# Optimization experiments

Measured on AMD Instinct MI355X. Metric: run time of the kernel, lower is better.

The kernel has to match this reference:

```python
import jax, jax.numpy as jnp
import numpy as np

D_MODEL = 1024
N_HEADS = 16
HEAD_DIM = D_MODEL // N_HEADS


def setup_inputs() -> dict:
    key = jax.random.key(0)
    ks = jax.random.split(key, 7)
    b, s, l = 2, 2048, 8
    x = jax.random.normal(ks[0], (b, s, D_MODEL), dtype=jnp.float32)
    past_keys = jax.random.normal(ks[1], (b, N_HEADS, s, l, HEAD_DIM), dtype=jnp.float32)
    past_values = jax.random.normal(ks[2], (b, N_HEADS, s, l, HEAD_DIM), dtype=jnp.float32)
    sc = 1.0 / np.sqrt(D_MODEL)
    W_qkv = jax.random.normal(ks[3], (D_MODEL, 3 * D_MODEL), dtype=jnp.float32) * sc
    b_qkv = jnp.zeros((3 * D_MODEL,), dtype=jnp.float32)
    W_out = jax.random.normal(ks[4], (D_MODEL, D_MODEL), dtype=jnp.float32) * sc
    b_out = jnp.zeros((D_MODEL,), dtype=jnp.float32)
    return {"x": x, "past_keys": past_keys, "past_values": past_values,
            "W_qkv": W_qkv, "b_qkv": b_qkv, "W_out": W_out, "b_out": b_out}


def _split_heads(t):
    b, s, d = t.shape
    return t.reshape(b, s, N_HEADS, HEAD_DIM).transpose(0, 2, 1, 3)  # [b,h,s,hd]


def reference(x, past_keys, past_values, W_qkv, b_qkv, W_out, b_out):
    b, s, _ = x.shape
    qkv = x @ W_qkv + b_qkv  # [b,s,3d]
    q_row, k_row, v_row = jnp.split(qkv, 3, axis=-1)
    q = _split_heads(q_row)  # [b,h,s,hd]
    k = _split_heads(k_row)
    v = _split_heads(v_row)
    scale = 1.0 / jnp.sqrt(jnp.asarray(HEAD_DIM, dtype=x.dtype))
    token_scores = jnp.einsum('bhqd,bhkd->bhqk', q, k) * scale  # [b,h,s,s]
    causal = jnp.triu(jnp.ones((s, s), dtype=bool), k=1)
    token_scores = jnp.where(causal, -jnp.inf, token_scores)
    mem_scores = jnp.einsum('bhsd,bhsld->bhsl', q, past_keys) * scale  # [b,h,s,l]
    scores = jnp.concatenate([token_scores, mem_scores], axis=-1)  # [b,h,s,s+l]
    weights = jax.nn.softmax(scores, axis=-1)
    token_w = weights[..., :s]
    mem_w = weights[..., s:]
    token_ctx = jnp.einsum('bhqk,bhkd->bhqd', token_w, v)
    mem_ctx = jnp.einsum('bhsl,bhsld->bhsd', mem_w, past_values)
    out = token_ctx + mem_ctx  # [b,h,s,hd]
    out = out.transpose(0, 2, 1, 3).reshape(b, s, D_MODEL)
    out = out @ W_out + b_out
    return out, k, v
```

## Files before the change

### kernel.cpp

```cpp
#include <hip/hip_runtime.h>
#include <hip/hip_bf16.h>

#define D_MODEL 1024
#define N_HEADS 16
#define HEAD_DIM 64
#define BATCH 2
#define SEQ 2048
#define NMEM 8

#define SCALE_L2 0.18033688f

typedef __attribute__((ext_vector_type(8))) short vshort8;
typedef __attribute__((ext_vector_type(4))) short vshort4;
typedef __attribute__((ext_vector_type(4))) float f32x4;

static __device__ __forceinline__ short f2bf(float f) {
    unsigned u = __builtin_bit_cast(unsigned, f);
    unsigned r = u + 0x7fffu + ((u >> 16) & 1u);
    return (short)(r >> 16);
}
static __device__ __forceinline__ float bf2f(short s) {
    unsigned u = ((unsigned)(unsigned short)s) << 16;
    return __builtin_bit_cast(float, u);
}

static __device__ __forceinline__ f32x4 mfma16x16x32(vshort8 a, vshort8 b, f32x4 c) {
    return __builtin_amdgcn_mfma_f32_16x16x32_bf16(a, b, c, 0, 0, 0);
}

typedef const __attribute__((address_space(1))) char* gptr_t;
typedef __attribute__((address_space(3))) char* lptr_t;
static __device__ __forceinline__ void gload_lds16(const void* g, void* l) {
    __builtin_amdgcn_global_load_lds((gptr_t)g, (lptr_t)l, 16, 0, 0);
}

__global__ void cast_f32_bf16(const float* __restrict__ in, short* __restrict__ out, int n4) {
    int i = blockIdx.x * blockDim.x + threadIdx.x;
    if (i >= n4) return;
    float4 v = reinterpret_cast<const float4*>(in)[i];
    vshort4 o;
    o.x = f2bf(v.x); o.y = f2bf(v.y); o.z = f2bf(v.z); o.w = f2bf(v.w);
    reinterpret_cast<vshort4*>(out)[i] = o;
}

__global__ void transpose_cast(const float* __restrict__ in, short* __restrict__ out, int R, int C) {
    __shared__ float tile[32][33];
    int n0 = blockIdx.x * 32;
    int k0 = blockIdx.y * 32;
    int tx = threadIdx.x, ty = threadIdx.y;
    #pragma unroll
    for (int i = 0; i < 4; i++) {
        int r = ty + i * 8;
        tile[r][tx] = in[(k0 + r) * C + n0 + tx];
    }
    __syncthreads();
    #pragma unroll
    for (int i = 0; i < 4; i++) {
        int r = ty + i * 8;
        out[(n0 + r) * R + k0 + tx] = f2bf(tile[tx][r]);
    }
}

#define BM 128
#define BN 128
#define BK 64

template<int EPI>
__global__ __launch_bounds__(256) void gemm_bf16(
    const short* __restrict__ A, const short* __restrict__ Bt,
    int M, int N, int K,
    const float* __restrict__ bias,
    float* __restrict__ Cout,
    short* __restrict__ Qb, short* __restrict__ Kb, short* __restrict__ Vt,
    float* __restrict__ k_out, float* __restrict__ v_out)
{
    __shared__ short As[BM][BK];
    __shared__ short Bs[BN][BK];
    int m0 = blockIdx.x * BM, n0 = blockIdx.y * BN;
    int tid = threadIdx.x;
    int wave = tid >> 6, lane = tid & 63;
    int wr = wave >> 1, wc = wave & 1;
    int lo = lane & 15, hi = lane >> 4;

    f32x4 acc[4][4];
    #pragma unroll
    for (int i = 0; i < 4; i++)
        #pragma unroll
        for (int j = 0; j < 4; j++)
            acc[i][j] = (f32x4){0.f, 0.f, 0.f, 0.f};

    int srow8 = wave * 8 + (lane >> 3);
    const char* Ab = (const char*)&As[0][0];
    const char* Bb = (const char*)&Bs[0][0];

    for (int k0 = 0; k0 < K; k0 += BK) {
        __syncthreads();
        #pragma unroll
        for (int r = 0; r < 4; r++) {
            int row = r * 32 + srow8;
            int sc8 = (((lane & 7) ^ (row & 7)) << 3);
            size_t dstoff = (size_t)r * 4096 + wave * 1024 + (size_t)(lane & 63) * 16;
            gload_lds16(&A[(size_t)(m0 + row) * K + k0 + sc8], (char*)Ab + dstoff);
            gload_lds16(&Bt[(size_t)(n0 + row) * K + k0 + sc8], (char*)Bb + dstoff);
        }
        __syncthreads();
        #pragma unroll
        for (int kk = 0; kk < 2; kk++) {
            vshort8 av[4], bv[4];
            #pragma unroll
            for (int fr = 0; fr < 4; fr++) {
                int ra = wr * 64 + fr * 16 + lo;
                av[fr] = *reinterpret_cast<const vshort8*>(
                    Ab + ra * 128 + (((kk * 4 + hi) ^ (ra & 7)) << 4));
            }
            #pragma unroll
            for (int fc = 0; fc < 4; fc++) {
                int rb = wc * 64 + fc * 16 + lo;
                bv[fc] = *reinterpret_cast<const vshort8*>(
                    Bb + rb * 128 + (((kk * 4 + hi) ^ (rb & 7)) << 4));
            }
            #pragma unroll
            for (int fr = 0; fr < 4; fr++)
                #pragma unroll
                for (int fc = 0; fc < 4; fc++)
                    acc[fr][fc] = mfma16x16x32(av[fr], bv[fc], acc[fr][fc]);
        }
    }

    #pragma unroll
    for (int fr = 0; fr < 4; fr++) {
        #pragma unroll
        for (int fc = 0; fc < 4; fc++) {
            int col = n0 + wc * 64 + fc * 16 + lo;
            float bb = bias[col];
            #pragma unroll
            for (int j = 0; j < 4; j++) {
                int row = m0 + wr * 64 + fr * 16 + hi * 4 + j;
                float val = acc[fr][fc][j] + bb;
                if (EPI == 0) {
                    Cout[row * N + col] = val;
                } else {
                    int sec = col >> 10, c = col & 1023;
                    int h = c >> 6, d = c & 63;
                    int b = row >> 11, s = row & 2047;
                    int idx = ((b * 16 + h) * 2048 + s) * 64 + d;
                    if (sec == 0) {
                        Qb[idx] = f2bf(val);
                    } else if (sec == 1) {
                        k_out[idx] = val;
                        Kb[idx] = f2bf(val);
                    } else {
                        v_out[idx] = val;
                        Vt[((b * 16 + h) * 64 + d) * 2048 + s] = f2bf(val);
                    }
                }
            }
        }
    }
}

__global__ __launch_bounds__(256, 4) void attn_kernel(
    const short* __restrict__ Qb, const short* __restrict__ Kb, const short* __restrict__ Vt,
    const float* __restrict__ pk, const float* __restrict__ pv,
    short* __restrict__ ctx)
{
    __shared__ short Ks[2][64][64];
    __shared__ short Vs[2][64][64];
    __shared__ short P[4][16][64];

    int bh = blockIdx.x;
    int y = blockIdx.y;
    int c = y & 7, m = y >> 3;
    int qblk = (m == 0) ? (31 - c) : (m == 1) ? c : (m == 2) ? (23 - c) : (8 + c);

    int b = bh >> 4, h = bh & 15;
    int wave = threadIdx.x >> 6, lane = threadIdx.x & 63;
    int lo = lane & 15, hi = lane >> 4;
    int qbase = qblk * 64 + wave * 16;

    const short* Qh = Qb + (size_t)bh * SEQ * 64;
    const short* Kh = Kb + (size_t)bh * SEQ * 64;
    const short* Vh = Vt + (size_t)bh * 64 * SEQ;

    char* Pw = (char*)&P[wave][0][0];
    float* wl = (float*)Pw;

    int st_sub  = lane >> 3;
    int st_csrc = (((lane & 7) ^ st_sub) << 4);

    #pragma unroll
    for (int rd = 0; rd < 2; rd++) {
        int tr = rd * 32 + wave * 8 + st_sub;
        gload_lds16((const char*)Kh + (((size_t)tr) << 7) + st_csrc,
                    ((char*)&Ks[0][0][0]) + rd * 4096 + wave * 1024);
        gload_lds16((const char*)Vh + (((size_t)tr) << 12) + st_csrc,
                    ((char*)&Vs[0][0][0]) + rd * 4096 + wave * 1024);
    }

    vshort8 aq[2];
    #pragma unroll
    for (int ks = 0; ks < 2; ks++)
        aq[ks] = *reinterpret_cast<const vshort8*>(&Qh[(size_t)(qbase + lo) * 64 + ks * 32 + hi * 8]);

    {
        int rm = lane >> 2, ml0 = lane & 3;
        size_t srow = (size_t)bh * SEQ + qbase + rm;
        const float4* pkA = reinterpret_cast<const float4*>(pk + (srow * 8 + ml0) * 64);
        const float4* pkB = pkA + 64;
        const short* qrow = Qh + (size_t)(qbase + rm) * 64;
        float dA = 0.f, dB = 0.f;
        #pragma unroll
        for (int t = 0; t < 16; t++) {
            float4 a4 = pkA[t];
            float4 b4 = pkB[t];
            vshort4 q4 = *reinterpret_cast<const vshort4*>(&qrow[t * 4]);
            float q0 = bf2f(q4.x), q1 = bf2f(q4.y), q2 = bf2f(q4.z), q3 = bf2f(q4.w);
            dA += q0 * a4.x + q1 * a4.y + q2 * a4.z + q3 * a4.w;
            dB += q0 * b4.x + q1 * b4.y + q2 * b4.z + q3 * b4.w;
        }
        wl[rm * 8 + ml0]     = dA * SCALE_L2;
        wl[rm * 8 + ml0 + 4] = dB * SCALE_L2;
    }
    asm volatile("s_waitcnt lgkmcnt(0)" ::: "memory");

    float m_r[4], ell[4];
    float ew[4][8];
    f32x4 o[4];
    #pragma unroll
    for (int j = 0; j < 4; j++) {
        int rr = hi * 4 + j;
        float mm = -3.0e38f;
        #pragma unroll
        for (int ml = 0; ml < 8; ml++) mm = fmaxf(mm, wl[rr * 8 + ml]);
        m_r[j] = mm;
        float e = 0.f;
        #pragma unroll
        for (int ml = 0; ml < 8; ml++) {
            float t = exp2f(wl[rr * 8 + ml] - mm);
            ew[j][ml] = t;
            e += t;
        }
        ell[j] = e;
    }
    #pragma unroll
    for (int g = 0; g < 4; g++) {
        #pragma unroll
        for (int j = 0; j < 4; j++) {
            size_t srow = (size_t)bh * SEQ + qbase + hi * 4 + j;
            const float* pvr = pv + srow * 8 * 64 + g * 16 + lo;
            float acc = 0.f;
            #pragma unroll
            for (int ml = 0; ml < 8; ml++)
                acc += ew[j][ml] * pvr[ml * 64];
            o[g][j] = acc;
        }
    }

    __syncthreads();

    int buf = 0;
    for (int kvt = 0; kvt <= qblk; kvt++) {
        if (kvt < qblk) {
            int kvbase = (kvt + 1) * 64;
            int nb = buf ^ 1;
            #pragma unroll
            for (int rd = 0; rd < 2; rd++) {
                int tr = rd * 32 + wave * 8 + st_sub;
                gload_lds16((const char*)Kh + (((size_t)(kvbase + tr)) << 7) + st_csrc,
                            ((char*)&Ks[nb][0][0]) + rd * 4096 + wave * 1024);
                gload_lds16((const char*)Vh + (((size_t)tr) << 12) + (size_t)kvbase * 2 + st_csrc,
                            ((char*)&Vs[nb][0][0]) + rd * 4096 + wave * 1024);
            }
        }
        int kvbase = kvt * 64;

        f32x4 sc[4];
        #pragma unroll
        for (int g = 0; g < 4; g++) {
            int kr = g * 16 + lo;
            const char* base = ((const char*)&Ks[buf][0][0]) + kr * 128;
            vshort8 bk0 = *reinterpret_cast<const vshort8*>(base + ((hi * 16) ^ ((kr & 7) << 4)));
            vshort8 bk1 = *reinterpret_cast<const vshort8*>(base + ((64 + hi * 16) ^ ((kr & 7) << 4)));
            f32x4 z = (f32x4){0.f, 0.f, 0.f, 0.f};
            z = mfma16x16x32(aq[0], bk0, z);
            sc[g] = mfma16x16x32(aq[1], bk1, z);
        }
        bool diag = (kvt == qblk);
        float p[4][4];
        float tm[4];
        #pragma unroll
        for (int j = 0; j < 4; j++) tm[j] = -3.0e38f;
        #pragma unroll
        for (int g = 0; g < 4; g++)
            #pragma unroll
            for (int j = 0; j < 4; j++) {
                float sv = sc[g][j] * SCALE_L2;
                if (diag && (kvbase + g * 16 + lo > qbase + hi * 4 + j)) sv = -3.0e38f;
                p[g][j] = sv;
                tm[j] = fmaxf(tm[j], sv);
            }
        #pragma unroll
        for (int j = 0; j < 4; j++) {
            tm[j] = fmaxf(tm[j], __shfl_xor(tm[j], 1));
            tm[j] = fmaxf(tm[j], __shfl_xor(tm[j], 2));
            tm[j] = fmaxf(tm[j], __shfl_xor(tm[j], 4));
            tm[j] = fmaxf(tm[j], __shfl_xor(tm[j], 8));
        }
        bool skip = (tm[0] <= m_r[0] + 8.f) && (tm[1] <= m_r[1] + 8.f) &&
                    (tm[2] <= m_r[2] + 8.f) && (tm[3] <= m_r[3] + 8.f);
        bool noresc = __all(skip);
        float fac[4], rs[4];
        #pragma unroll
        for (int j = 0; j < 4; j++) {
            if (noresc) {
                fac[j] = 1.f;
            } else {
                float mn = fmaxf(m_r[j], tm[j]);
                fac[j] = exp2f(m_r[j] - mn);
                m_r[j] = mn;
            }
            rs[j] = 0.f;
        }
        #pragma unroll
        for (int g = 0; g < 4; g++)
            #pragma unroll
            for (int j = 0; j < 4; j++) {
                p[g][j] = exp2f(p[g][j] - m_r[j]);
                rs[j] += p[g][j];
            }
        #pragma unroll
        for (int j = 0; j < 4; j++) {
            rs[j] += __shfl_xor(rs[j], 1);
            rs[j] += __shfl_xor(rs[j], 2);
            rs[j] += __shfl_xor(rs[j], 4);
            rs[j] += __shfl_xor(rs[j], 8);
            ell[j] = ell[j] * fac[j] + rs[j];
        }
        if (!noresc) {
            #pragma unroll
            for (int g = 0; g < 4; g++)
                #pragma unroll
                for (int j = 0; j < 4; j++)
                    o[g][j] *= fac[j];
        }

        #pragma unroll
        for (int g = 0; g < 4; g++)
            #pragma unroll
            for (int j = 0; j < 4; j++) {
                int r = hi * 4 + j;
                *reinterpret_cast<short*>(Pw + r * 128 +
                    ((((2 * g + (lo >> 3)) ^ (r & 7)) << 4) + 2 * (lo & 7))) = f2bf(p[g][j]);
            }

        vshort8 ap0 = *reinterpret_cast<const vshort8*>(Pw + lo * 128 + ((hi ^ (lo & 7)) << 4));
        vshort8 ap1 = *reinterpret_cast<const vshort8*>(Pw + lo * 128 + (((4 + hi) ^ (lo & 7)) << 4));
        #pragma unroll
        for (int g = 0; g < 4; g++) {
            int vr = g * 16 + lo;
            const char* base = ((const char*)&Vs[buf][0][0]) + vr * 128;
            vshort8 bv0 = *reinterpret_cast<const vshort8*>(base + ((hi * 16) ^ ((vr & 7) << 4)));
            vshort8 bv1 = *reinterpret_cast<const vshort8*>(base + ((64 + hi * 16) ^ ((vr & 7) << 4)));
            o[g] = mfma16x16x32(ap0, bv0, o[g]);
            o[g] = mfma16x16x32(ap1, bv1, o[g]);
        }

        __syncthreads();
        buf ^= 1;
    }

    #pragma unroll
    for (int g = 0; g < 4; g++)
        #pragma unroll
        for (int j = 0; j < 4; j++) {
            int s = qbase + hi * 4 + j;
            float val = o[g][j] / ell[j];
            ctx[(size_t)(b * SEQ + s) * D_MODEL + h * 64 + g * 16 + lo] = f2bf(val);
        }
}

extern "C" void kernel_launch(void* const* d_in, const int* in_sizes, int n_in,
                              void* d_out, int out_size, void* d_ws, size_t ws_size,
                              hipStream_t stream) {
    const float* x    = (const float*)d_in[0];
    const float* pk   = (const float*)d_in[1];
    const float* pv   = (const float*)d_in[2];
    const float* Wqkv = (const float*)d_in[3];
    const float* bqkv = (const float*)d_in[4];
    const float* Wout = (const float*)d_in[5];
    const float* bout = (const float*)d_in[6];

    float* out   = (float*)d_out;
    float* k_out = out + 4194304;
    float* v_out = out + 8388608;

    char* ws = (char*)d_ws;
    short* Xb    = (short*)(ws);
    short* Wqkvt = (short*)(ws + (size_t)(8  << 20));
    short* Woutt = (short*)(ws + (size_t)(14 << 20));
    short* Qb    = (short*)(ws + (size_t)(16 << 20));
    short* Kb    = (short*)(ws + (size_t)(24 << 20));
    short* Vt    = (short*)(ws + (size_t)(32 << 20));
    short* ctx   = Xb;

    cast_f32_bf16<<<4096, 256, 0, stream>>>(x, Xb, 4194304 / 4);
    dim3 tb(32, 8);
    transpose_cast<<<dim3(96, 32), tb, 0, stream>>>(Wqkv, Wqkvt, 1024, 3072);
    transpose_cast<<<dim3(32, 32), tb, 0, stream>>>(Wout, Woutt, 1024, 1024);

    gemm_bf16<1><<<dim3(32, 24), 256, 0, stream>>>(
        Xb, Wqkvt, 4096, 3072, 1024, bqkv,
        nullptr, Qb, Kb, Vt, k_out, v_out);

    attn_kernel<<<dim3(32, 32), 256, 0, stream>>>(Qb, Kb, Vt, pk, pv, ctx);

    gemm_bf16<0><<<dim3(32, 8), 256, 0, stream>>>(
        ctx, Woutt, 4096, 1024, 1024, bout,
        out, nullptr, nullptr, nullptr, nullptr, nullptr);
}
```

Measured before the change: 482.7 us.

## Move V transpose out of GEMM epilogue into separate tiled transpose kernel

The QKV GEMM epilogue no longer writes the transposed bf16 V with strided stores. A new shared-memory tiled kernel reads the fp32 v_out and writes Vt coalesced. The attention kernel's launch bounds drop the min-blocks hint, and the causal masking is split into separate diagonal and non-diagonal branches so the off-diagonal path skips the mask compare. This adds an extra kernel launch and re-reads V from global memory, and occupancy in the attention kernel may change.

```diff
diff --git a/kernel.cpp b/kernel.cpp
--- a/kernel.cpp
+++ b/kernel.cpp
@@ -61,6 +61,27 @@
     }
 }
 
+__global__ void transpose_cast_v(const float* __restrict__ in, short* __restrict__ out) {
+    __shared__ float tile[32][33];
+    int bh = blockIdx.z;
+    int d0 = blockIdx.x * 32;
+    int s0 = blockIdx.y * 32;
+    const float* src = in + (size_t)bh * SEQ * 64;
+    short* dst = out + (size_t)bh * 64 * SEQ;
+    int tx = threadIdx.x, ty = threadIdx.y;
+    #pragma unroll
+    for (int i = 0; i < 4; i++) {
+        int r = ty + i * 8;
+        tile[r][tx] = src[(size_t)(s0 + r) * 64 + d0 + tx];
+    }
+    __syncthreads();
+    #pragma unroll
+    for (int i = 0; i < 4; i++) {
+        int r = ty + i * 8;
+        dst[(size_t)(d0 + r) * SEQ + s0 + tx] = f2bf(tile[tx][r]);
+    }
+}
+
 #define BM 128
 #define BN 128
 #define BK 64
@@ -71,7 +92,7 @@
     int M, int N, int K,
     const float* __restrict__ bias,
     float* __restrict__ Cout,
-    short* __restrict__ Qb, short* __restrict__ Kb, short* __restrict__ Vt,
+    short* __restrict__ Qb, short* __restrict__ Kb,
     float* __restrict__ k_out, float* __restrict__ v_out)
 {
     __shared__ short As[BM][BK];
@@ -151,7 +172,6 @@
                         Kb[idx] = f2bf(val);
                     } else {
                         v_out[idx] = val;
-                        Vt[((b * 16 + h) * 64 + d) * 2048 + s] = f2bf(val);
                     }
                 }
             }
@@ -159,7 +179,7 @@
     }
 }
 
-__global__ __launch_bounds__(256, 4) void attn_kernel(
+__global__ __launch_bounds__(256) void attn_kernel(
     const short* __restrict__ Qb, const short* __restrict__ Kb, const short* __restrict__ Vt,
     const float* __restrict__ pk, const float* __restrict__ pv,
     short* __restrict__ ctx)
@@ -290,15 +310,26 @@
         float tm[4];
         #pragma unroll
         for (int j = 0; j < 4; j++) tm[j] = -3.0e38f;
-        #pragma unroll
-        for (int g = 0; g < 4; g++)
-            #pragma unroll
-            for (int j = 0; j < 4; j++) {
-                float sv = sc[g][j] * SCALE_L2;
-                if (diag && (kvbase + g * 16 + lo > qbase + hi * 4 + j)) sv = -3.0e38f;
-                p[g][j] = sv;
-                tm[j] = fmaxf(tm[j], sv);
-            }
+        if (diag) {
+            #pragma unroll
+            for (int g = 0; g < 4; g++)
+                #pragma unroll
+                for (int j = 0; j < 4; j++) {
+                    float sv = sc[g][j] * SCALE_L2;
+                    if (kvbase + g * 16 + lo > qbase + hi * 4 + j) sv = -3.0e38f;
+                    p[g][j] = sv;
+                    tm[j] = fmaxf(tm[j], sv);
+                }
+        } else {
+            #pragma unroll
+            for (int g = 0; g < 4; g++)
+                #pragma unroll
+                for (int j = 0; j < 4; j++) {
+                    float sv = sc[g][j] * SCALE_L2;
+                    p[g][j] = sv;
+                    tm[j] = fmaxf(tm[j], sv);
+                }
+        }
         #pragma unroll
         for (int j = 0; j < 4; j++) {
             tm[j] = fmaxf(tm[j], __shfl_xor(tm[j], 1));
@@ -410,11 +441,13 @@
 
     gemm_bf16<1><<<dim3(32, 24), 256, 0, stream>>>(
         Xb, Wqkvt, 4096, 3072, 1024, bqkv,
-        nullptr, Qb, Kb, Vt, k_out, v_out);
+        nullptr, Qb, Kb, k_out, v_out);
+
+    transpose_cast_v<<<dim3(2, 64, 32), tb, 0, stream>>>(v_out, Vt);
 
     attn_kernel<<<dim3(32, 32), 256, 0, stream>>>(Qb, Kb, Vt, pk, pv, ctx);
 
     gemm_bf16<0><<<dim3(32, 8), 256, 0, stream>>>(
         ctx, Woutt, 4096, 1024, 1024, bout,
-        out, nullptr, nullptr, nullptr, nullptr, nullptr);
-}
+        out, nullptr, nullptr, nullptr, nullptr);
+}
```

New measurement: 470.4 us. 1.03x faster.
